# Kernel optimization log

Measured on AMD Instinct MI355X. Metric: run time of the kernel, lower is better.

Reference implementation:

```python
import jax, jax.numpy as jnp
import numpy as np

LMAX = 6
NUM_COEFFS = (LMAX + 1) ** 2  # 49
REPEATS = np.array([2 * l + 1 for l in range(LMAX + 1)])  # coefficients per degree


def so3_linear(x, w, b):
    """Block-diagonal per-degree linear: x [N, 49, Cin], w [lmax+1, Cin, Cout], b [Cout].
    Bias is added only to the degree-0 (scalar) coefficient."""
    w_exp = jnp.repeat(w, REPEATS, axis=0)  # [49, Cin, Cout]
    out = jnp.einsum('nic,ico->nio', x, w_exp)
    return out.at[:, 0, :].add(b)


def setup_inputs() -> dict:
    key = jax.random.key(0)
    ks = jax.random.split(key, 10)
    N, C, H = 1024, 128, 256
    res = 18
    s = 0.05
    return {
        'node_feats': jax.random.normal(ks[0], (N, NUM_COEFFS, C), jnp.float32),
        'w1': jax.random.normal(ks[1], (LMAX + 1, C, H), jnp.float32) * s,
        'b1': jnp.zeros((H,), jnp.float32),
        'w2': jax.random.normal(ks[2], (LMAX + 1, H, C), jnp.float32) * s,
        'b2': jnp.zeros((C,), jnp.float32),
        'ws': jax.random.normal(ks[3], (C, H), jnp.float32) * s,
        'bs': jnp.zeros((H,), jnp.float32),
        'g1': jax.random.normal(ks[4], (H, H), jnp.float32) * s,
        'g2': jax.random.normal(ks[5], (H, H), jnp.float32) * s,
        'g3': jax.random.normal(ks[6], (H, H), jnp.float32) * s,
        'to_grid_mat': jax.random.normal(ks[7], (res, res, NUM_COEFFS), jnp.float32) * s,
        'from_grid_mat': jax.random.normal(ks[8], (res, res, NUM_COEFFS), jnp.float32) * s,
    }


def reference(node_feats, w1, b1, w2, b2, ws, bs, g1, g2, g3, to_grid_mat, from_grid_mat):
    # separable-S2 scalar gating branch: MLP on the l=0 coefficient  [N,1,H]
    gating = jax.nn.silu(jnp.einsum('nic,ch->nih', node_feats[:, 0:1], ws) + bs)
    # SO3 linear 1  [N,49,H]
    x = so3_linear(node_feats, w1, b1)
    # spherical harmonics -> grid  [N, beta, alpha, H]
    grid = jnp.einsum('bai,nih->nbah', to_grid_mat, x)
    # grid MLP (bias-free) with SiLU between layers
    grid = jax.nn.silu(jnp.einsum('nbah,hk->nbak', grid, g1))
    grid = jax.nn.silu(jnp.einsum('nbak,km->nbam', grid, g2))
    grid = jnp.einsum('nbam,mh->nbah', grid, g3)
    # grid -> spherical harmonics  [N,49,H]
    x = jnp.einsum('bai,nbah->nih', from_grid_mat, grid)
    # separable S2: replace l=0 component with gated scalars
    x = jnp.concatenate((gating, x[:, 1:]), axis=1)
    # SO3 linear 2  [N,49,C_out]
    return so3_linear(x, w2, b2)
```

## Files before the change

### kernel.cpp

```cpp
#include <hip/hip_runtime.h>
#include <hip/hip_bf16.h>

typedef __attribute__((ext_vector_type(8))) short bf16x8;
typedef __attribute__((ext_vector_type(4))) float f32x4;

#define MFMA(a,b,c) __builtin_amdgcn_mfma_f32_16x16x32_bf16((a),(b),(c),0,0,0)

#define WS_W1T 0
#define WS_W2T 229376
#define WS_G1T 458752
#define WS_TGP 655360
#define WS_FGT 679936
#define WS_TOTAL 704512

__device__ __forceinline__ ushort f2b(float f) {
  __hip_bfloat16 h = __float2bfloat16(f);
  ushort u; __builtin_memcpy(&u, &h, 2); return u;
}
__device__ __forceinline__ float silu_f(float x) { return x / (1.f + __expf(-x)); }
__device__ __forceinline__ bf16x8 ld8(const ushort* p) {
  return *reinterpret_cast<const bf16x8*>(p);
}
__device__ __forceinline__ ushort4 pk4(float a, float b, float c, float d) {
  return make_ushort4(f2b(a), f2b(b), f2b(c), f2b(d));
}

__global__ void prep_kernel(const float* __restrict__ w1, const float* __restrict__ w2,
                            const float* __restrict__ g1, const float* __restrict__ g2,
                            const float* __restrict__ g3, const float* __restrict__ tg,
                            const float* __restrict__ fg, ushort* __restrict__ o) {
  int idx = blockIdx.x * blockDim.x + threadIdx.x;
  if (idx >= WS_TOTAL) return;
  float v;
  if (idx < WS_W2T) {
    int l = idx >> 15, rem = idx & 32767, h = rem >> 7, c = rem & 127;
    v = w1[(l << 15) + c * 256 + h];
  } else if (idx < WS_G1T) {
    int j = idx - WS_W2T;
    int l = j >> 15, rem = j & 32767, oo = rem >> 8, h = rem & 255;
    v = w2[(l << 15) + h * 128 + oo];
  } else if (idx < WS_TGP) {
    int j = idx - WS_G1T;
    int m = j >> 16, r = j & 65535, n2 = r >> 8, k = r & 255;
    const float* g = (m == 0) ? g1 : ((m == 1) ? g2 : g3);
    v = g[k * 256 + n2];
  } else if (idx < WS_FGT) {
    int j = idx - WS_TGP, r = j >> 6, i2 = j & 63;
    v = (r < 324 && i2 < 49) ? tg[r * 49 + i2] : 0.f;
  } else {
    int j = idx - WS_FGT, i2 = j / 384, r = j % 384;
    v = (i2 < 49 && r < 324) ? fg[r * 49 + i2] : 0.f;
  }
  o[idx] = f2b(v);
}

__global__ __launch_bounds__(512, 1) void ffn_main(
    const float* __restrict__ nf, const float* __restrict__ b1,
    const float* __restrict__ b2, const float* __restrict__ wsg,
    const float* __restrict__ bs, const ushort* __restrict__ wbf,
    float* __restrict__ out)
{
  __shared__ __align__(16) ushort sm[69120];
  ushort* s_G   = sm;
  ushort* s_GT  = sm + 33792;
  ushort* s_xbT = sm + 33792;
  float*  s_gat = reinterpret_cast<float*>(sm + 68608);
  ushort* s_nf  = s_G;
  ushort* s_xo  = s_G;

  const int tid  = threadIdx.x;
  const int lane = tid & 63;
  const int wv   = tid >> 6;
  const int lr   = lane & 15;
  const int lk   = lane >> 4;

  const float* nfp = nf + (size_t)blockIdx.x * 6272;

  {
    uint4 z = {0,0,0,0};
    for (int idx = tid; idx < 2304; idx += 512)
      *reinterpret_cast<uint4*>(&s_xbT[idx * 8]) = z;
    for (int idx = tid; idx < 52 * 32; idx += 512) {
      int r = idx >> 5, c4 = (idx & 31) << 2;
      float4 v = (r < 49) ? *reinterpret_cast<const float4*>(nfp + (r << 7) + c4)
                          : make_float4(0.f, 0.f, 0.f, 0.f);
      *reinterpret_cast<ushort4*>(&s_nf[r * 136 + c4]) = pk4(v.x, v.y, v.z, v.w);
    }
    if (tid < 256) {
      float a = bs[tid];
      #pragma unroll 4
      for (int c = 0; c < 128; ++c) a = fmaf(nfp[c], wsg[(c << 8) + tid], a);
      s_gat[tid] = silu_f(a);
    }
  }
  __syncthreads();

  {
    const ushort* w1T = wbf + WS_W1T;
    #pragma unroll 1
    for (int l = 0; l < 7; ++l) {
      f32x4 a0 = {0.f,0.f,0.f,0.f}, a1 = {0.f,0.f,0.f,0.f};
      const int arow = l * l + lr;
      const ushort* bb = w1T + (l << 15);
      #pragma unroll
      for (int ks = 0; ks < 4; ++ks) {
        bf16x8 af  = ld8(&s_nf[arow * 136 + ks * 32 + lk * 8]);
        bf16x8 bf0 = ld8(bb + ((wv * 32 + lr) << 7) + ks * 32 + lk * 8);
        bf16x8 bf1 = ld8(bb + ((wv * 32 + 16 + lr) << 7) + ks * 32 + lk * 8);
        a0 = MFMA(af, bf0, a0);
        a1 = MFMA(af, bf1, a1);
      }
      const int nv = 2 * l + 1;
      #pragma unroll
      for (int reg = 0; reg < 4; ++reg) {
        int il = lk * 4 + reg;
        if (il < nv) {
          int ig = l * l + il;
          int h0 = wv * 32 + lr, h1 = h0 + 16;
          s_xbT[h0 * 72 + ig] = f2b(a0[reg] + (ig == 0 ? b1[h0] : 0.f));
          s_xbT[h1 * 72 + ig] = f2b(a1[reg] + (ig == 0 ? b1[h1] : 0.f));
        }
      }
    }
  }
  __syncthreads();

  bf16x8 xbf[2][2];
  #pragma unroll
  for (int nt = 0; nt < 2; ++nt)
    #pragma unroll
    for (int ks = 0; ks < 2; ++ks)
      xbf[nt][ks] = ld8(&s_xbT[(wv * 32 + nt * 16 + lr) * 72 + ks * 32 + lk * 8]);

  f32x4 xo[4][2];
  #pragma unroll
  for (int mt = 0; mt < 4; ++mt)
    #pragma unroll
    for (int nt = 0; nt < 2; ++nt) xo[mt][nt] = (f32x4){0.f,0.f,0.f,0.f};

  const ushort* tgP = wbf + WS_TGP;
  const ushort* fgT = wbf + WS_FGT;

  #pragma unroll 1
  for (int ch = 0; ch < 3; ++ch) {
    {
      f32x4 c[8][2];
      #pragma unroll
      for (int mt = 0; mt < 8; ++mt)
        #pragma unroll
        for (int nt = 0; nt < 2; ++nt) c[mt][nt] = (f32x4){0.f,0.f,0.f,0.f};
      #pragma unroll
      for (int ks = 0; ks < 2; ++ks) {
        bf16x8 atg[8];
        #pragma unroll
        for (int mt = 0; mt < 8; ++mt)
          atg[mt] = ld8(tgP + ((ch * 128 + mt * 16 + lr) << 6) + ks * 32 + lk * 8);
        #pragma unroll
        for (int mt = 0; mt < 8; ++mt)
          #pragma unroll
          for (int nt = 0; nt < 2; ++nt) c[mt][nt] = MFMA(xbf[nt][ks], atg[mt], c[mt][nt]);
      }
      #pragma unroll
      for (int mt = 0; mt < 8; ++mt)
        #pragma unroll
        for (int nt = 0; nt < 2; ++nt)
          *reinterpret_cast<ushort4*>(&s_G[(mt * 16 + lr) * 264 + wv * 32 + nt * 16 + lk * 4]) =
              pk4(c[mt][nt][0], c[mt][nt][1], c[mt][nt][2], c[mt][nt][3]);
    }
    __syncthreads();

    #pragma unroll 1
    for (int pass = 0; pass < 2; ++pass) {
      const ushort* gT = wbf + WS_G1T + (pass << 16);
      f32x4 c[8][2];
      #pragma unroll
      for (int mt = 0; mt < 8; ++mt)
        #pragma unroll
        for (int nt = 0; nt < 2; ++nt) c[mt][nt] = (f32x4){0.f,0.f,0.f,0.f};
      #pragma unroll
      for (int ks = 0; ks < 8; ++ks) {
        bf16x8 bstr[2];
        #pragma unroll
        for (int nt = 0; nt < 2; ++nt)
          bstr[nt] = ld8(gT + ((wv * 32 + nt * 16 + lr) << 8) + ks * 32 + lk * 8);
        bf16x8 af[8];
        #pragma unroll
        for (int mt = 0; mt < 8; ++mt)
          af[mt] = ld8(&s_G[(mt * 16 + lr) * 264 + ks * 32 + lk * 8]);
        #pragma unroll
        for (int mt = 0; mt < 8; ++mt)
          #pragma unroll
          for (int nt = 0; nt < 2; ++nt) c[mt][nt] = MFMA(bstr[nt], af[mt], c[mt][nt]);
      }
      __syncthreads();
      #pragma unroll
      for (int mt = 0; mt < 8; ++mt)
        #pragma unroll
        for (int nt = 0; nt < 2; ++nt)
          *reinterpret_cast<ushort4*>(&s_G[(mt * 16 + lr) * 264 + wv * 32 + nt * 16 + lk * 4]) =
              pk4(silu_f(c[mt][nt][0]), silu_f(c[mt][nt][1]),
                  silu_f(c[mt][nt][2]), silu_f(c[mt][nt][3]));
      __syncthreads();
    }

    {
      const ushort* g3T = wbf + WS_G1T + 131072;
      f32x4 c[8][2];
      #pragma unroll
      for (int mt = 0; mt < 8; ++mt)
        #pragma unroll
        for (int nt = 0; nt < 2; ++nt) c[mt][nt] = (f32x4){0.f,0.f,0.f,0.f};
      #pragma unroll
      for (int ks = 0; ks < 8; ++ks) {
        bf16x8 bstr[2];
        #pragma unroll
        for (int nt = 0; nt < 2; ++nt)
          bstr[nt] = ld8(g3T + ((wv * 32 + nt * 16 + lr) << 8) + ks * 32 + lk * 8);
        bf16x8 af[8];
        #pragma unroll
        for (int mt = 0; mt < 8; ++mt)
          af[mt] = ld8(&s_G[(mt * 16 + lr) * 264 + ks * 32 + lk * 8]);
        #pragma unroll
        for (int mt = 0; mt < 8; ++mt)
          #pragma unroll
          for (int nt = 0; nt < 2; ++nt) c[mt][nt] = MFMA(af[mt], bstr[nt], c[mt][nt]);
      }
      __syncthreads();
      #pragma unroll
      for (int mt = 0; mt < 8; ++mt)
        #pragma unroll
        for (int nt = 0; nt < 2; ++nt) {
          int h = wv * 32 + nt * 16 + lr;
          *reinterpret_cast<ushort4*>(&s_GT[h * 136 + mt * 16 + lk * 4]) =
              pk4(c[mt][nt][0], c[mt][nt][1], c[mt][nt][2], c[mt][nt][3]);
        }
    }
    __syncthreads();

    {
      #pragma unroll
      for (int ks = 0; ks < 4; ++ks) {
        bf16x8 afg[4];
        #pragma unroll
        for (int mt = 0; mt < 4; ++mt)
          afg[mt] = ld8(fgT + (mt * 16 + lr) * 384 + ch * 128 + ks * 32 + lk * 8);
        bf16x8 bfr[2];
        #pragma unroll
        for (int nt = 0; nt < 2; ++nt)
          bfr[nt] = ld8(&s_GT[(wv * 32 + nt * 16 + lr) * 136 + ks * 32 + lk * 8]);
        #pragma unroll
        for (int mt = 0; mt < 4; ++mt)
          #pragma unroll
          for (int nt = 0; nt < 2; ++nt) xo[mt][nt] = MFMA(bfr[nt], afg[mt], xo[mt][nt]);
      }
    }
  }

  #pragma unroll
  for (int mt = 0; mt < 4; ++mt)
    #pragma unroll
    for (int nt = 0; nt < 2; ++nt)
      *reinterpret_cast<ushort4*>(&s_xo[(mt * 16 + lr) * 264 + wv * 32 + nt * 16 + lk * 4]) =
          pk4(xo[mt][nt][0], xo[mt][nt][1], xo[mt][nt][2], xo[mt][nt][3]);
  __syncthreads();
  if (tid < 256) s_xo[tid] = f2b(s_gat[tid]);
  __syncthreads();

  {
    const ushort* w2T = wbf + WS_W2T;
    float* outp = out + (size_t)blockIdx.x * 6272;
    const float4 bb2 = *reinterpret_cast<const float4*>(b2 + wv * 16 + lk * 4);
    #pragma unroll 1
    for (int l = 0; l < 7; ++l) {
      f32x4 acc = {0.f,0.f,0.f,0.f};
      const ushort* bb = w2T + (l << 15);
      const int arow = l * l + lr;
      #pragma unroll
      for (int ks = 0; ks < 8; ++ks) {
        bf16x8 xf = ld8(&s_xo[arow * 264 + ks * 32 + lk * 8]);
        bf16x8 wf = ld8(bb + ((wv * 16 + lr) << 8) + ks * 32 + lk * 8);
        acc = MFMA(wf, xf, acc);
      }
      if (lr < 2 * l + 1) {
        int ig = l * l + lr;
        float4 v = make_float4(acc[0], acc[1], acc[2], acc[3]);
        if (ig == 0) { v.x += bb2.x; v.y += bb2.y; v.z += bb2.z; v.w += bb2.w; }
        *reinterpret_cast<float4*>(outp + (ig << 7) + wv * 16 + lk * 4) = v;
      }
    }
  }
}

extern "C" void kernel_launch(void* const* d_in, const int* in_sizes, int n_in,
                              void* d_out, int out_size, void* d_ws, size_t ws_size,
                              hipStream_t stream) {
  const float* nf  = (const float*)d_in[0];
  const float* w1  = (const float*)d_in[1];
  const float* b1  = (const float*)d_in[2];
  const float* w2  = (const float*)d_in[3];
  const float* b2  = (const float*)d_in[4];
  const float* wsg = (const float*)d_in[5];
  const float* bs  = (const float*)d_in[6];
  const float* g1  = (const float*)d_in[7];
  const float* g2  = (const float*)d_in[8];
  const float* g3  = (const float*)d_in[9];
  const float* tg  = (const float*)d_in[10];
  const float* fg  = (const float*)d_in[11];
  ushort* wbf = (ushort*)d_ws;
  float* out = (float*)d_out;

  prep_kernel<<<(WS_TOTAL + 255) / 256, 256, 0, stream>>>(w1, w2, g1, g2, g3, tg, fg, wbf);
  ffn_main<<<1024, 512, 0, stream>>>(nf, b1, b2, wsg, bs, wbf, out);
}
```

Before: 555.9 us.

## Swizzle LDS grid buffers and ping-pong between two buffers across MLP layers

Replaces the padded row-stride LDS layout for the grid activations with an XOR-swizzled layout, which removes the padding while aiming to keep ds_read_b128 and the packed writes free of bank conflicts. The two grid-MLP passes are unrolled and alternate between two LDS buffers (Ga/Gb). This drops the barrier that came before each in-place write-back. The gating scalar now stays in a register instead of a separate LDS slot. The trade-off is extra address arithmetic per LDS access, plus a dependence on correct buffer aliasing between stages.

```diff
diff --git a/kernel.cpp b/kernel.cpp
--- a/kernel.cpp
+++ b/kernel.cpp
@@ -23,6 +23,12 @@
 }
 __device__ __forceinline__ ushort4 pk4(float a, float b, float c, float d) {
   return make_ushort4(f2b(a), f2b(b), f2b(c), f2b(d));
+}
+__device__ __forceinline__ ushort* swzG(ushort* base, int row, int colByte) {
+  return (ushort*)((char*)base + row * 512 + (((colByte >> 4) ^ (row & 7)) << 4) + (colByte & 15));
+}
+__device__ __forceinline__ ushort* swzT(ushort* base, int row, int colByte) {
+  return (ushort*)((char*)base + row * 256 + (((colByte >> 4) ^ (row & 7)) << 4) + (colByte & 15));
 }
 
 __global__ void prep_kernel(const float* __restrict__ w1, const float* __restrict__ w2,
@@ -60,13 +66,12 @@
     const float* __restrict__ bs, const ushort* __restrict__ wbf,
     float* __restrict__ out)
 {
-  __shared__ __align__(16) ushort sm[69120];
-  ushort* s_G   = sm;
-  ushort* s_GT  = sm + 33792;
-  ushort* s_xbT = sm + 33792;
-  float*  s_gat = reinterpret_cast<float*>(sm + 68608);
-  ushort* s_nf  = s_G;
-  ushort* s_xo  = s_G;
+  __shared__ __align__(16) ushort sm[65536];
+  ushort* Ga = sm;
+  ushort* Gb = sm + 32768;
+  ushort* s_nf  = Ga;
+  ushort* s_xbT = Gb;
+  ushort* s_xo  = Ga;
 
   const int tid  = threadIdx.x;
   const int lane = tid & 63;
@@ -76,6 +81,7 @@
 
   const float* nfp = nf + (size_t)blockIdx.x * 6272;
 
+  float gat = 0.f;
   {
     uint4 z = {0,0,0,0};
     for (int idx = tid; idx < 2304; idx += 512)
@@ -90,7 +96,7 @@
       float a = bs[tid];
       #pragma unroll 4
       for (int c = 0; c < 128; ++c) a = fmaf(nfp[c], wsg[(c << 8) + tid], a);
-      s_gat[tid] = silu_f(a);
+      gat = silu_f(a);
     }
   }
   __syncthreads();
@@ -164,14 +170,13 @@
       for (int mt = 0; mt < 8; ++mt)
         #pragma unroll
         for (int nt = 0; nt < 2; ++nt)
-          *reinterpret_cast<ushort4*>(&s_G[(mt * 16 + lr) * 264 + wv * 32 + nt * 16 + lk * 4]) =
+          *reinterpret_cast<ushort4*>(swzG(Ga, mt * 16 + lr, wv * 64 + nt * 32 + lk * 8)) =
               pk4(c[mt][nt][0], c[mt][nt][1], c[mt][nt][2], c[mt][nt][3]);
     }
     __syncthreads();
 
-    #pragma unroll 1
-    for (int pass = 0; pass < 2; ++pass) {
-      const ushort* gT = wbf + WS_G1T + (pass << 16);
+    {
+      const ushort* gT = wbf + WS_G1T;
       f32x4 c[8][2];
       #pragma unroll
       for (int mt = 0; mt < 8; ++mt)
@@ -186,25 +191,24 @@
         bf16x8 af[8];
         #pragma unroll
         for (int mt = 0; mt < 8; ++mt)
-          af[mt] = ld8(&s_G[(mt * 16 + lr) * 264 + ks * 32 + lk * 8]);
+          af[mt] = ld8(swzG(Ga, mt * 16 + lr, ks * 64 + lk * 16));
         #pragma unroll
         for (int mt = 0; mt < 8; ++mt)
           #pragma unroll
           for (int nt = 0; nt < 2; ++nt) c[mt][nt] = MFMA(bstr[nt], af[mt], c[mt][nt]);
       }
-      __syncthreads();
-      #pragma unroll
-      for (int mt = 0; mt < 8; ++mt)
-        #pragma unroll
-        for (int nt = 0; nt < 2; ++nt)
-          *reinterpret_cast<ushort4*>(&s_G[(mt * 16 + lr) * 264 + wv * 32 + nt * 16 + lk * 4]) =
+      #pragma unroll
+      for (int mt = 0; mt < 8; ++mt)
+        #pragma unroll
+        for (int nt = 0; nt < 2; ++nt)
+          *reinterpret_cast<ushort4*>(swzG(Gb, mt * 16 + lr, wv * 64 + nt * 32 + lk * 8)) =
               pk4(silu_f(c[mt][nt][0]), silu_f(c[mt][nt][1]),
                   silu_f(c[mt][nt][2]), silu_f(c[mt][nt][3]));
-      __syncthreads();
-    }
-
-    {
-      const ushort* g3T = wbf + WS_G1T + 131072;
+    }
+    __syncthreads();
+
+    {
+      const ushort* gT = wbf + WS_G1T + 65536;
       f32x4 c[8][2];
       #pragma unroll
       for (int mt = 0; mt < 8; ++mt)
@@ -215,11 +219,43 @@
         bf16x8 bstr[2];
         #pragma unroll
         for (int nt = 0; nt < 2; ++nt)
-          bstr[nt] = ld8(g3T + ((wv * 32 + nt * 16 + lr) << 8) + ks * 32 + lk * 8);
+          bstr[nt] = ld8(gT + ((wv * 32 + nt * 16 + lr) << 8) + ks * 32 + lk * 8);
         bf16x8 af[8];
         #pragma unroll
         for (int mt = 0; mt < 8; ++mt)
-          af[mt] = ld8(&s_G[(mt * 16 + lr) * 264 + ks * 32 + lk * 8]);
+          af[mt] = ld8(swzG(Gb, mt * 16 + lr, ks * 64 + lk * 16));
+        #pragma unroll
+        for (int mt = 0; mt < 8; ++mt)
+          #pragma unroll
+          for (int nt = 0; nt < 2; ++nt) c[mt][nt] = MFMA(bstr[nt], af[mt], c[mt][nt]);
+      }
+      #pragma unroll
+      for (int mt = 0; mt < 8; ++mt)
+        #pragma unroll
+        for (int nt = 0; nt < 2; ++nt)
+          *reinterpret_cast<ushort4*>(swzG(Ga, mt * 16 + lr, wv * 64 + nt * 32 + lk * 8)) =
+              pk4(silu_f(c[mt][nt][0]), silu_f(c[mt][nt][1]),
+                  silu_f(c[mt][nt][2]), silu_f(c[mt][nt][3]));
+    }
+    __syncthreads();
+
+    {
+      const ushort* gT = wbf + WS_G1T + 131072;
+      f32x4 c[8][2];
+      #pragma unroll
+      for (int mt = 0; mt < 8; ++mt)
+        #pragma unroll
+        for (int nt = 0; nt < 2; ++nt) c[mt][nt] = (f32x4){0.f,0.f,0.f,0.f};
+      #pragma unroll
+      for (int ks = 0; ks < 8; ++ks) {
+        bf16x8 bstr[2];
+        #pragma unroll
+        for (int nt = 0; nt < 2; ++nt)
+          bstr[nt] = ld8(gT + ((wv * 32 + nt * 16 + lr) << 8) + ks * 32 + lk * 8);
+        bf16x8 af[8];
+        #pragma unroll
+        for (int mt = 0; mt < 8; ++mt)
+          af[mt] = ld8(swzG(Ga, mt * 16 + lr, ks * 64 + lk * 16));
         #pragma unroll
         for (int mt = 0; mt < 8; ++mt)
           #pragma unroll
@@ -231,7 +267,7 @@
         #pragma unroll
         for (int nt = 0; nt < 2; ++nt) {
           int h = wv * 32 + nt * 16 + lr;
-          *reinterpret_cast<ushort4*>(&s_GT[h * 136 + mt * 16 + lk * 4]) =
+          *reinterpret_cast<ushort4*>(swzT(Gb, h, mt * 32 + lk * 8)) =
               pk4(c[mt][nt][0], c[mt][nt][1], c[mt][nt][2], c[mt][nt][3]);
         }
     }
@@ -247,7 +283,7 @@
         bf16x8 bfr[2];
         #pragma unroll
         for (int nt = 0; nt < 2; ++nt)
-          bfr[nt] = ld8(&s_GT[(wv * 32 + nt * 16 + lr) * 136 + ks * 32 + lk * 8]);
+          bfr[nt] = ld8(swzT(Gb, wv * 32 + nt * 16 + lr, ks * 64 + lk * 16));
         #pragma unroll
         for (int mt = 0; mt < 4; ++mt)
           #pragma unroll
@@ -260,10 +296,10 @@
   for (int mt = 0; mt < 4; ++mt)
     #pragma unroll
     for (int nt = 0; nt < 2; ++nt)
-      *reinterpret_cast<ushort4*>(&s_xo[(mt * 16 + lr) * 264 + wv * 32 + nt * 16 + lk * 4]) =
+      *reinterpret_cast<ushort4*>(swzG(Ga, mt * 16 + lr, wv * 64 + nt * 32 + lk * 8)) =
           pk4(xo[mt][nt][0], xo[mt][nt][1], xo[mt][nt][2], xo[mt][nt][3]);
   __syncthreads();
-  if (tid < 256) s_xo[tid] = f2b(s_gat[tid]);
+  if (tid < 256) s_xo[tid] = f2b(gat);
   __syncthreads();
 
   {
@@ -277,7 +313,7 @@
       const int arow = l * l + lr;
       #pragma unroll
       for (int ks = 0; ks < 8; ++ks) {
-        bf16x8 xf = ld8(&s_xo[arow * 264 + ks * 32 + lk * 8]);
+        bf16x8 xf = ld8(swzG(Ga, arow, ks * 64 + lk * 16));
         bf16x8 wf = ld8(bb + ((wv * 16 + lr) << 8) + ks * 32 + lk * 8);
         acc = MFMA(wf, xf, acc);
       }
```

Result: slower. 751.3 us (+35.1%).
